# Kernel tuning notes

Measured on AMD Instinct MI355X. Metric: run time of the kernel, lower is better.

## Reference

```python
import jax, jax.numpy as jnp
from jax import lax
import numpy as np

PH, PW = 5, 5      # patch_shape; forced to 5x5 by the (batch, F, 27) reshape in AdaptiveConv
F = 32             # adaptive conv output channels
SCALE = 4          # super-resolution upscale factor


def conv2d(x, w, b, padding):
    # x: NCHW, w: OIHW
    y = lax.conv_general_dilated(x, w, (1, 1), padding,
                                 dimension_numbers=('NCHW', 'OIHW', 'NCHW'))
    return y + b[None, :, None, None]


def space_to_batch(x):
    # non-overlapping PHxPW tiles, order (batch, tile_row, tile_col) like the torch loops
    B, C, H, W = x.shape
    hn, wn = H // PH, W // PW
    p = x.reshape(B, C, hn, PH, wn, PW).transpose(0, 2, 4, 1, 3, 5)
    return p.reshape(B * hn * wn, C, PH, PW), (B, hn, wn)


def batch_to_space(p, meta):
    B, hn, wn = meta
    C = p.shape[1]
    out = p.reshape(B, hn, wn, C, PH, PW).transpose(0, 3, 1, 4, 2, 5)
    return out.reshape(B, C, hn * PH, wn * PW)


def unfold3(x):
    # torch F.unfold(x, 3, padding=1): (N, C*9, L) channel-major (c, kh, kw); return (N, L, C*9)
    N, C, H, W = x.shape
    xp = jnp.pad(x, ((0, 0), (0, 0), (1, 1), (1, 1)))
    cols = jnp.stack([xp[:, :, i:i + H, j:j + W]
                      for i in range(3) for j in range(3)], axis=2)  # (N, C, 9, H, W)
    return cols.reshape(N, C * 9, H * W).transpose(0, 2, 1)


def pixel_shuffle(x, r):
    B, Cr2, H, W = x.shape
    C = Cr2 // (r * r)
    return (x.reshape(B, C, r, r, H, W)
             .transpose(0, 1, 4, 2, 5, 3)
             .reshape(B, C, H * r, W * r))


def setup_inputs() -> dict:
    key = jax.random.key(0)
    ks = jax.random.split(key, 13)
    rn = lambda k, shape, s=0.05: jax.random.normal(k, shape, jnp.float32) * s
    return dict(
        x=jax.random.normal(ks[0], (2, 3, 360, 640), jnp.float32),
        w_feat=rn(ks[1], (256, 3, 3, 3)),        b_feat=rn(ks[2], (256,)),
        w_kern=rn(ks[3], (27 * F, 256, 3, 3)),   b_kern=rn(ks[4], (27 * F,)),
        w_badp=rn(ks[5], (F, 256, 3, 3)),        b_badp=rn(ks[6], (F,)),
        w1=rn(ks[7], (128, F, 5, 5)),            b1=rn(ks[8], (128,)),
        w2=rn(ks[9], (32, 128, 3, 3)),           b2=rn(ks[10], (32,)),
        w3=rn(ks[11], (3 * SCALE * SCALE, 32, 3, 3)), b3=rn(ks[12], (3 * SCALE * SCALE,)),
    )


def reference(x, w_feat, b_feat, w_kern, b_kern, w_badp, b_badp,
              w1, b1, w2, b2, w3, b3):
    patches, meta = space_to_batch(x)                        # (N, 3, 5, 5)
    N = patches.shape[0]
    # AdaptiveConv: per-patch dynamic 3x3 conv
    feat = jax.nn.relu(conv2d(patches, w_feat, b_feat, 'VALID'))   # (N, 256, 3, 3)
    kern = conv2d(feat, w_kern, b_kern, 'VALID')                   # (N, 27F, 1, 1)
    kern = kern.reshape(N, F, 27).transpose(0, 2, 1)               # (N, 27, F)
    xu = unfold3(patches)                                          # (N, 25, 27)
    out = jnp.einsum('nlk,nkf->nlf', xu, kern)                     # (N, 25, F)
    out = out.transpose(0, 2, 1).reshape(N, F, PH, PW)
    bias = conv2d(feat, w_badp, b_badp, 'VALID')                   # (N, F, 1, 1)
    out = jax.nn.relu(out + bias)
    sp = batch_to_space(out, meta)                                 # (B, F, H, W)
    # RegularConv stack
    h = jax.nn.relu(conv2d(sp, w1, b1, 'SAME'))
    h = jax.nn.relu(conv2d(h, w2, b2, 'SAME'))
    h = conv2d(h, w3, b3, 'SAME')                                  # (B, 3*r*r, H, W)
    return pixel_shuffle(h, SCALE)                                 # (B, 3, H*r, W*r)
```

## Files before the change

### kernel.cpp

```cpp
#include <hip/hip_runtime.h>
#include <stdint.h>

typedef unsigned short ushort;
typedef __bf16 bf16x8 __attribute__((ext_vector_type(8)));
typedef float f32x4 __attribute__((ext_vector_type(4)));
typedef ushort ushort8 __attribute__((ext_vector_type(8)));

__device__ __forceinline__ float bf2f(ushort u) {
  union { unsigned int i; float f; } v; v.i = ((unsigned int)u) << 16; return v.f;
}
__device__ __forceinline__ ushort f2bf(float f) {
  union { float f; unsigned int i; } v; v.f = f;
  unsigned int r = v.i + 0x7fffu + ((v.i >> 16) & 1u);
  return (ushort)(r >> 16);
}
__device__ __forceinline__ void glds16(const ushort* g, ushort* l) {
  __builtin_amdgcn_global_load_lds(
      (const __attribute__((address_space(1))) void*)g,
      (__attribute__((address_space(3))) void*)l, 16, 0, 0);
}

__global__ __launch_bounds__(256) void pack_kernel(
    const float* __restrict__ w_kern, const float* __restrict__ b_kern,
    const float* __restrict__ w_badp, const float* __restrict__ b_badp,
    ushort* __restrict__ Bt, float* __restrict__ bias896) {
  int idx = blockIdx.x * 256 + threadIdx.x;
  const int total = 896 * 2304;
  if (idx < total) {
    int o = idx / 2304, k = idx - o * 2304;
    int c = k & 255, pos = k >> 8;
    float v = (o < 864) ? w_kern[(o * 256 + c) * 9 + pos]
                        : w_badp[((o - 864) * 256 + c) * 9 + pos];
    Bt[idx] = f2bf(v);
  } else if (idx < total + 896) {
    int o = idx - total;
    bias896[o] = (o < 864) ? b_kern[o] : b_badp[o - 864];
  }
}

__global__ __launch_bounds__(256) void pack2_kernel(
    const float* __restrict__ w1, const float* __restrict__ w2,
    const float* __restrict__ w3, ushort* __restrict__ wp1,
    ushort* __restrict__ wp2, ushort* __restrict__ wp3) {
  int idx = blockIdx.x * 256 + threadIdx.x;
  if (idx < 102400) {
    int t = idx >> 12, rm = idx & 4095, o = rm >> 5, c = rm & 31;
    wp1[idx] = f2bf(w1[(o * 32 + c) * 25 + t]);
  } else if (idx < 102400 + 36864) {
    int j = idx - 102400;
    int t = j >> 12, rm = j & 4095, o = rm >> 7, c = rm & 127;
    wp2[j] = f2bf(w2[(o * 128 + c) * 9 + t]);
  } else if (idx < 102400 + 36864 + 13824) {
    int j = idx - 139264;
    int t = j / 1536, rm = j - t * 1536, o = rm >> 5, c = rm & 31;
    wp3[j] = f2bf(w3[(o * 32 + c) * 9 + t]);
  }
}

__global__ __launch_bounds__(256) void feat_kernel(
    const float* __restrict__ x, const float* __restrict__ w_feat,
    const float* __restrict__ b_feat, ushort* __restrict__ feat) {
  __shared__ float xp[4][3][5][5];
  const int t = threadIdx.x;
  const int n0 = blockIdx.x * 4;
  for (int e = t; e < 300; e += 256) {
    int p = e / 75, rem = e - p * 75;
    int ci = rem / 25, r = rem - ci * 25, i = r / 5, j = r - i * 5;
    int n = n0 + p;
    int b = n / 9216, ph = (n >> 7) % 72, pw = n & 127;
    xp[p][ci][i][j] = x[((b * 3 + ci) * 360 + ph * 5 + i) * 640 + pw * 5 + j];
  }
  float wf[27];
#pragma unroll
  for (int m = 0; m < 27; ++m) wf[m] = w_feat[t * 27 + m];
  const float bv = b_feat[t];
  __syncthreads();
  for (int p = 0; p < 4; ++p) {
    ushort* dst = feat + (size_t)(n0 + p) * 2304 + t;
#pragma unroll
    for (int pi = 0; pi < 3; ++pi)
#pragma unroll
      for (int pj = 0; pj < 3; ++pj) {
        float acc = bv;
#pragma unroll
        for (int ci = 0; ci < 3; ++ci)
#pragma unroll
          for (int ki = 0; ki < 3; ++ki)
#pragma unroll
            for (int kj = 0; kj < 3; ++kj)
              acc = fmaf(xp[p][ci][pi + ki][pj + kj], wf[ci * 9 + ki * 3 + kj], acc);
        dst[(pi * 3 + pj) * 256] = f2bf(fmaxf(acc, 0.f));
      }
  }
}

__global__ __launch_bounds__(256) void gemm_kernel(
    const ushort* __restrict__ A, const ushort* __restrict__ Bt,
    const float* __restrict__ bias, ushort* __restrict__ C) {
  const int K = 2304, N = 896;
  __shared__ __align__(16) ushort lA[128 * 32];
  __shared__ __align__(16) ushort lB[128 * 32];
  const int m0 = blockIdx.x * 128, n0 = blockIdx.y * 128;
  const int t = threadIdx.x;
  const int lane = t & 63, wave = t >> 6;
  const int wm = wave >> 1, wn = wave & 1;
  f32x4 acc[4][4] = {};
  const ushort* gA = A + (size_t)(m0 + (t >> 2)) * K + (t & 3) * 8;
  const ushort* gB = Bt + (size_t)(n0 + (t >> 2)) * K + (t & 3) * 8;
  ushort* dA0 = &lA[wave * 512];
  ushort* dA1 = &lA[2048 + wave * 512];
  ushort* dB0 = &lB[wave * 512];
  ushort* dB1 = &lB[2048 + wave * 512];
  const int aoff = (wm * 64 + (lane & 15)) * 32 + (lane >> 4) * 8;
  const int boff = (wn * 64 + (lane & 15)) * 32 + (lane >> 4) * 8;
  for (int kt = 0; kt < K; kt += 32) {
    __syncthreads();
    glds16(gA + kt, dA0);
    glds16(gA + 64 * K + kt, dA1);
    glds16(gB + kt, dB0);
    glds16(gB + 64 * K + kt, dB1);
    __syncthreads();
    bf16x8 af[4], bfr[4];
#pragma unroll
    for (int mi = 0; mi < 4; ++mi) {
      ushort8 tmp = *(const ushort8*)(&lA[aoff + mi * 512]);
      af[mi] = __builtin_bit_cast(bf16x8, tmp);
    }
#pragma unroll
    for (int ni = 0; ni < 4; ++ni) {
      ushort8 tmp = *(const ushort8*)(&lB[boff + ni * 512]);
      bfr[ni] = __builtin_bit_cast(bf16x8, tmp);
    }
#pragma unroll
    for (int mi = 0; mi < 4; ++mi)
#pragma unroll
      for (int ni = 0; ni < 4; ++ni)
        acc[mi][ni] = __builtin_amdgcn_mfma_f32_16x16x32_bf16(af[mi], bfr[ni], acc[mi][ni], 0, 0, 0);
  }
#pragma unroll
  for (int ni = 0; ni < 4; ++ni) {
    int col = n0 + wn * 64 + ni * 16 + (lane & 15);
    float bv = bias[col];
#pragma unroll
    for (int mi = 0; mi < 4; ++mi) {
      int row0 = m0 + wm * 64 + mi * 16 + (lane >> 4) * 4;
#pragma unroll
      for (int r = 0; r < 4; ++r)
        C[(size_t)(row0 + r) * N + col] = f2bf(acc[mi][ni][r] + bv);
    }
  }
}

__global__ __launch_bounds__(256) void apply_kernel(
    const float* __restrict__ x, const ushort* __restrict__ kernbias,
    ushort* __restrict__ sp) {
  __shared__ float xp[8][3][7][7];
  __shared__ ushort outl[8][32][25];
  const int t = threadIdx.x;
  const int n0 = blockIdx.x * 8;
  const int b = n0 / 9216, ph = (n0 >> 7) % 72, pw0 = n0 & 127;
  for (int e = t; e < 8 * 3 * 49; e += 256) ((float*)xp)[e] = 0.f;
  __syncthreads();
  for (int e = t; e < 600; e += 256) {
    int p = e / 75, rem = e - p * 75;
    int ci = rem / 25, r = rem - ci * 25, i = r / 5, j = r - i * 5;
    xp[p][ci][i + 1][j + 1] = x[((b * 3 + ci) * 360 + ph * 5 + i) * 640 + (pw0 + p) * 5 + j];
  }
  __syncthreads();
  const int p = t >> 5, f = t & 31;
  const int n = n0 + p;
  float kk[27];
#pragma unroll
  for (int k = 0; k < 27; ++k) kk[k] = bf2f(kernbias[(size_t)n * 896 + f * 27 + k]);
  const float bv = bf2f(kernbias[(size_t)n * 896 + 864 + f]);
  for (int l = 0; l < 25; ++l) {
    int li = l / 5, lj = l - li * 5;
    float s = bv;
#pragma unroll
    for (int k = 0; k < 27; ++k) {
      int ci = k / 9, rm = k - ci * 9, ki = rm / 3, kj = rm - ki * 3;
      s = fmaf(xp[p][ci][li + ki][lj + kj], kk[k], s);
    }
    outl[p][f][l] = f2bf(fmaxf(s, 0.f));
  }
  __syncthreads();
  for (int e = t; e < 6400; e += 256) {
    int f2 = e & 31;
    int idx = e >> 5;
    int i = idx / 40, c40 = idx - i * 40;
    int pp = c40 / 5, j = c40 - pp * 5;
    sp[(((size_t)b * 360 + ph * 5 + i) * 640 + pw0 * 5 + c40) * 32 + f2] = outl[pp][f2][i * 5 + j];
  }
}

__global__ __launch_bounds__(512) void conv1_kernel(
    const ushort* __restrict__ sp, const ushort* __restrict__ wp1,
    const float* __restrict__ b1, ushort* __restrict__ h1) {
  __shared__ ushort8 lin[8 * 4 * 69];
  const int t = threadIdx.x;
  const int lane = t & 63, wave = t >> 6;
  const int wh = wave >> 1, wn = wave & 1;
  const int w0 = blockIdx.x * 64, h0 = blockIdx.y * 4, b = blockIdx.z;
  for (int u = t; u < 8 * 4 * 68; u += 512) {
    int c8 = u & 3, rest = u >> 2;
    int wx = rest % 68, r = rest / 68;
    int gh = h0 - 2 + r, gw = w0 - 2 + wx;
    ushort8 v = {};
    if ((unsigned)gh < 360u && (unsigned)gw < 640u)
      v = *(const ushort8*)(sp + (((size_t)b * 360 + gh) * 640 + gw) * 32 + c8 * 8);
    lin[(r * 4 + c8) * 69 + wx] = v;
  }
  __syncthreads();
  f32x4 acc[4][4] = {};
  const int abase = (lane >> 4) * 69 + (lane & 15);
  const ushort* wbase = wp1 + (wn * 64 + (lane & 15)) * 32 + (lane >> 4) * 8;
#pragma unroll 1
  for (int ki = 0; ki < 5; ++ki) {
#pragma unroll
    for (int kj = 0; kj < 5; ++kj) {
      const int tap = ki * 5 + kj;
      bf16x8 bfr[4];
#pragma unroll
      for (int nf = 0; nf < 4; ++nf) {
        ushort8 tmp = *(const ushort8*)(wbase + (size_t)tap * 4096 + nf * 512);
        bfr[nf] = __builtin_bit_cast(bf16x8, tmp);
      }
      bf16x8 afr[4];
#pragma unroll
      for (int mf = 0; mf < 4; ++mf)
        afr[mf] = __builtin_bit_cast(bf16x8, lin[(wh + ki) * 276 + abase + mf * 16 + kj]);
#pragma unroll
      for (int mf = 0; mf < 4; ++mf)
#pragma unroll
        for (int nf = 0; nf < 4; ++nf)
          acc[mf][nf] = __builtin_amdgcn_mfma_f32_16x16x32_bf16(afr[mf], bfr[nf], acc[mf][nf], 0, 0, 0);
    }
  }
  const int h = h0 + wh;
#pragma unroll
  for (int nf = 0; nf < 4; ++nf) {
    int oc = wn * 64 + nf * 16 + (lane & 15);
    float bv = b1[oc];
#pragma unroll
    for (int mf = 0; mf < 4; ++mf) {
      int w = w0 + mf * 16 + ((lane >> 4) << 2);
      size_t base = (((size_t)b * 360 + h) * 640 + w) * 128 + oc;
#pragma unroll
      for (int r = 0; r < 4; ++r)
        h1[base + (size_t)r * 128] = f2bf(fmaxf(acc[mf][nf][r] + bv, 0.f));
    }
  }
}

__device__ __forceinline__ void c2_load(ushort8* stg, const ushort* __restrict__ h1,
                                        int t, int b, int h0, int w0, int cb) {
#pragma unroll
  for (int j = 0; j < 7; ++j) {
    int u = t + j * 256;
    ushort8 v = {};
    if (u < 1584) {
      int r = u / 264, rem = u - r * 264;
      int c8 = rem / 66, wx = rem - c8 * 66;
      int gh = h0 - 1 + r, gw = w0 - 1 + wx;
      if ((unsigned)gh < 360u && (unsigned)gw < 640u)
        v = *(const ushort8*)(h1 + (((size_t)b * 360 + gh) * 640 + gw) * 128 + cb * 32 + c8 * 8);
    }
    stg[j] = v;
  }
}
__device__ __forceinline__ void c2_write(const ushort8* stg, ushort8* buf, int t) {
#pragma unroll
  for (int j = 0; j < 7; ++j) {
    int u = t + j * 256;
    if (u < 1584) {
      int r = u / 264, rem = u - r * 264;
      int c8 = rem / 66, wx = rem - c8 * 66;
      buf[c8 * 414 + r * 69 + wx] = stg[j];
    }
  }
}
__device__ __forceinline__ void c2_compute(const ushort8* buf, const ushort* __restrict__ wp2,
                                           int cb, int wave, int lp, int lk, f32x4 acc[4][2]) {
#pragma unroll
  for (int ki = 0; ki < 3; ++ki) {
    const int rb = lk * 414 + (wave + ki) * 69;
#pragma unroll
    for (int kj = 0; kj < 3; ++kj) {
      const int tap = ki * 3 + kj;
      bf16x8 bfr[2];
#pragma unroll
      for (int nf = 0; nf < 2; ++nf) {
        ushort8 tmp = *(const ushort8*)(wp2 + tap * 4096 + nf * 2048 + lp * 128 + cb * 32 + lk * 8);
        bfr[nf] = __builtin_bit_cast(bf16x8, tmp);
      }
      bf16x8 afr[4];
#pragma unroll
      for (int mf = 0; mf < 4; ++mf)
        afr[mf] = __builtin_bit_cast(bf16x8, buf[rb + lp + mf * 16 + kj]);
#pragma unroll
      for (int mf = 0; mf < 4; ++mf)
#pragma unroll
        for (int nf = 0; nf < 2; ++nf)
          acc[mf][nf] = __builtin_amdgcn_mfma_f32_16x16x32_bf16(afr[mf], bfr[nf], acc[mf][nf], 0, 0, 0);
    }
  }
}

__global__ __launch_bounds__(256) void conv2_kernel(
    const ushort* __restrict__ h1, const ushort* __restrict__ wp2,
    const float* __restrict__ b2, ushort* __restrict__ h2) {
  __shared__ ushort8 lin[2][4 * 414];
  const int t = threadIdx.x;
  const int lane = t & 63, wave = t >> 6;
  const int lp = lane & 15, lk = lane >> 4;
  const int w0 = blockIdx.x * 64, h0 = blockIdx.y * 4, b = blockIdx.z;
  f32x4 acc[4][2] = {};
  ushort8 stg[7];
  c2_load(stg, h1, t, b, h0, w0, 0);
#pragma unroll
  for (int it = 0; it < 5; ++it) {
    __syncthreads();
    if (it < 4) c2_write(stg, lin[it & 1], t);
    if (it < 3) c2_load(stg, h1, t, b, h0, w0, it + 1);
    if (it >= 1) c2_compute(lin[(it - 1) & 1], wp2, it - 1, wave, lp, lk, acc);
  }
  const int h = h0 + wave;
#pragma unroll
  for (int nf = 0; nf < 2; ++nf) {
    int oc = nf * 16 + lp;
    float bv = b2[oc];
#pragma unroll
    for (int mf = 0; mf < 4; ++mf) {
      int w = w0 + mf * 16 + lk * 4;
      size_t base = (((size_t)b * 360 + h) * 640 + w) * 32 + oc;
#pragma unroll
      for (int r = 0; r < 4; ++r)
        h2[base + (size_t)r * 32] = f2bf(fmaxf(acc[mf][nf][r] + bv, 0.f));
    }
  }
}

__global__ __launch_bounds__(256) void conv3_kernel(
    const ushort* __restrict__ h2, const ushort* __restrict__ wp3,
    const float* __restrict__ b3, float* __restrict__ out) {
  __shared__ ushort8 lin[4 * 4 * 67];
  const int t = threadIdx.x;
  const int lane = t & 63, wave = t >> 6;
  const int wh = wave & 1, wm = wave >> 1;
  const int w0 = blockIdx.x * 64, h0 = blockIdx.y * 2, b = blockIdx.z;
  for (int u = t; u < 4 * 4 * 66; u += 256) {
    int c8 = u & 3, rest = u >> 2;
    int wx = rest % 66, r = rest / 66;
    int gh = h0 - 1 + r, gw = w0 - 1 + wx;
    ushort8 v = {};
    if (gh >= 0 && gh < 360 && gw >= 0 && gw < 640)
      v = *(const ushort8*)(h2 + (((size_t)b * 360 + gh) * 640 + gw) * 32 + c8 * 8);
    lin[(r * 4 + c8) * 67 + wx] = v;
  }
  __syncthreads();
  f32x4 acc[2][3] = {};
  const int abase = (lane >> 4) * 67 + wm * 32 + (lane & 15);
  const ushort* wbase = wp3 + ((lane & 15)) * 32 + (lane >> 4) * 8;
#pragma unroll 1
  for (int ki = 0; ki < 3; ++ki) {
#pragma unroll
    for (int kj = 0; kj < 3; ++kj) {
      const int tap = ki * 3 + kj;
      bf16x8 bfr[3];
#pragma unroll
      for (int nf = 0; nf < 3; ++nf) {
        ushort8 tmp = *(const ushort8*)(wbase + (size_t)tap * 1536 + nf * 512);
        bfr[nf] = __builtin_bit_cast(bf16x8, tmp);
      }
      bf16x8 afr[2];
#pragma unroll
      for (int mf = 0; mf < 2; ++mf)
        afr[mf] = __builtin_bit_cast(bf16x8, lin[(wh + ki) * 268 + abase + mf * 16 + kj]);
#pragma unroll
      for (int mf = 0; mf < 2; ++mf)
#pragma unroll
        for (int nf = 0; nf < 3; ++nf)
          acc[mf][nf] = __builtin_amdgcn_mfma_f32_16x16x32_bf16(afr[mf], bfr[nf], acc[mf][nf], 0, 0, 0);
    }
  }
  const int h = h0 + wh;
#pragma unroll
  for (int nf = 0; nf < 3; ++nf) {
    int oc = nf * 16 + (lane & 15);
    float bv = b3[oc];
    int c = oc >> 4, r1 = (oc >> 2) & 3, r2 = oc & 3;
#pragma unroll
    for (int mf = 0; mf < 2; ++mf) {
      int wb = w0 + wm * 32 + mf * 16 + ((lane >> 4) << 2);
#pragma unroll
      for (int r = 0; r < 4; ++r) {
        int w = wb + r;
        out[(((size_t)b * 3 + c) * 1440 + h * 4 + r1) * 2560 + (size_t)w * 4 + r2] =
            acc[mf][nf][r] + bv;
      }
    }
  }
}

extern "C" void kernel_launch(void* const* d_in, const int* in_sizes, int n_in,
                              void* d_out, int out_size, void* d_ws, size_t ws_size,
                              hipStream_t stream) {
  const float* x      = (const float*)d_in[0];
  const float* w_feat = (const float*)d_in[1];
  const float* b_feat = (const float*)d_in[2];
  const float* w_kern = (const float*)d_in[3];
  const float* b_kern = (const float*)d_in[4];
  const float* w_badp = (const float*)d_in[5];
  const float* b_badp = (const float*)d_in[6];
  const float* w1 = (const float*)d_in[7];
  const float* b1 = (const float*)d_in[8];
  const float* w2 = (const float*)d_in[9];
  const float* b2 = (const float*)d_in[10];
  const float* w3 = (const float*)d_in[11];
  const float* b3 = (const float*)d_in[12];

  char* ws = (char*)d_ws;
  ushort* feat     = (ushort*)(ws);
  ushort* h1       = (ushort*)(ws);
  ushort* kernbias = (ushort*)(ws + 117964800);
  ushort* h2       = (ushort*)(ws + 117964800);
  ushort* wp1      = (ushort*)(ws + 147456000);
  ushort* wp2      = (ushort*)(ws + 147660800);
  ushort* wp3      = (ushort*)(ws + 147734528);
  ushort* sp       = (ushort*)(ws + 150994944);
  ushort* Bt       = (ushort*)(ws + 180486144);
  float*  bias896  = (float*)(ws + 184614912);

  pack_kernel<<<(896 * 2304 + 896 + 255) / 256, 256, 0, stream>>>(
      w_kern, b_kern, w_badp, b_badp, Bt, bias896);
  feat_kernel<<<4608, 256, 0, stream>>>(x, w_feat, b_feat, feat);
  gemm_kernel<<<dim3(144, 7), 256, 0, stream>>>(feat, Bt, bias896, kernbias);
  apply_kernel<<<2304, 256, 0, stream>>>(x, kernbias, sp);
  pack2_kernel<<<598, 256, 0, stream>>>(w1, w2, w3, wp1, wp2, wp3);
  conv1_kernel<<<dim3(10, 90, 2), 512, 0, stream>>>(sp, wp1, b1, h1);
  conv2_kernel<<<dim3(10, 90, 2), 256, 0, stream>>>(h1, wp2, b2, h2);
  conv3_kernel<<<dim3(10, 180, 2), 256, 0, stream>>>(h2, wp3, b3, (float*)d_out);
}
```

Baseline: 514.6 us.

## Swap MFMA operands for vectorized epilogue stores and prefetch conv1 weights

The MFMA operand order in conv1, conv2 and conv3 is swapped so each lane's accumulator holds four consecutive output channels. The epilogues can then write packed 4-element bf16 or float4 stores with vectorized bias loads, replacing scattered scalar 2-byte and 4-byte stores. Conv1 also double-buffers its per-tap weight fragments in registers, prefetching the next tap's weights while the current tap's MFMAs run, to hide global load latency. This costs extra registers in conv1 and relies on the transposed accumulator layout matching the new index math.

```diff
diff --git a/kernel.cpp b/kernel.cpp
--- a/kernel.cpp
+++ b/kernel.cpp
@@ -5,6 +5,7 @@
 typedef __bf16 bf16x8 __attribute__((ext_vector_type(8)));
 typedef float f32x4 __attribute__((ext_vector_type(4)));
 typedef ushort ushort8 __attribute__((ext_vector_type(8)));
+typedef ushort us4 __attribute__((ext_vector_type(4)));
 
 __device__ __forceinline__ float bf2f(ushort u) {
   union { unsigned int i; float f; } v; v.i = ((unsigned int)u) << 16; return v.f;
@@ -18,6 +19,9 @@
   __builtin_amdgcn_global_load_lds(
       (const __attribute__((address_space(1))) void*)g,
       (__attribute__((address_space(3))) void*)l, 16, 0, 0);
+}
+__device__ __forceinline__ bf16x8 ldw(const ushort* p) {
+  return __builtin_bit_cast(bf16x8, *(const ushort8*)p);
 }
 
 __global__ __launch_bounds__(256) void pack_kernel(
@@ -212,42 +216,51 @@
   }
   __syncthreads();
   f32x4 acc[4][4] = {};
-  const int abase = (lane >> 4) * 69 + (lane & 15);
-  const ushort* wbase = wp1 + (wn * 64 + (lane & 15)) * 32 + (lane >> 4) * 8;
+  const int lp = lane & 15, lk = lane >> 4;
+  const int abase0 = lk * 69 + lp;
+  const ushort* wb = wp1 + (wn * 64 + lp) * 32 + lk * 8;
+
+  bf16x8 wc[4], wx_[4];
+#pragma unroll
+  for (int nf = 0; nf < 4; ++nf) wc[nf] = ldw(wb + nf * 512);
+
+  auto do_tap = [&](int tp, const bf16x8* wr) {
+    int ki = (tp * 13) >> 6, kj = tp - ki * 5;
+    int ab = (wh + ki) * 276 + abase0 + kj;
+    bf16x8 afr[4];
+#pragma unroll
+    for (int mf = 0; mf < 4; ++mf)
+      afr[mf] = __builtin_bit_cast(bf16x8, lin[ab + mf * 16]);
+#pragma unroll
+    for (int mf = 0; mf < 4; ++mf)
+#pragma unroll
+      for (int nf = 0; nf < 4; ++nf)
+        acc[mf][nf] = __builtin_amdgcn_mfma_f32_16x16x32_bf16(wr[nf], afr[mf], acc[mf][nf], 0, 0, 0);
+  };
+
 #pragma unroll 1
-  for (int ki = 0; ki < 5; ++ki) {
-#pragma unroll
-    for (int kj = 0; kj < 5; ++kj) {
-      const int tap = ki * 5 + kj;
-      bf16x8 bfr[4];
-#pragma unroll
-      for (int nf = 0; nf < 4; ++nf) {
-        ushort8 tmp = *(const ushort8*)(wbase + (size_t)tap * 4096 + nf * 512);
-        bfr[nf] = __builtin_bit_cast(bf16x8, tmp);
-      }
-      bf16x8 afr[4];
-#pragma unroll
-      for (int mf = 0; mf < 4; ++mf)
-        afr[mf] = __builtin_bit_cast(bf16x8, lin[(wh + ki) * 276 + abase + mf * 16 + kj]);
-#pragma unroll
-      for (int mf = 0; mf < 4; ++mf)
-#pragma unroll
-        for (int nf = 0; nf < 4; ++nf)
-          acc[mf][nf] = __builtin_amdgcn_mfma_f32_16x16x32_bf16(afr[mf], bfr[nf], acc[mf][nf], 0, 0, 0);
-    }
-  }
+  for (int tp = 0; tp < 24; tp += 2) {
+#pragma unroll
+    for (int nf = 0; nf < 4; ++nf) wx_[nf] = ldw(wb + (tp + 1) * 4096 + nf * 512);
+    do_tap(tp, wc);
+#pragma unroll
+    for (int nf = 0; nf < 4; ++nf) wc[nf] = ldw(wb + (tp + 2) * 4096 + nf * 512);
+    do_tap(tp + 1, wx_);
+  }
+  do_tap(24, wc);
+
   const int h = h0 + wh;
 #pragma unroll
   for (int nf = 0; nf < 4; ++nf) {
-    int oc = wn * 64 + nf * 16 + (lane & 15);
-    float bv = b1[oc];
+    const int oc0 = wn * 64 + nf * 16 + lk * 4;
+    f32x4 bv = *(const f32x4*)(b1 + oc0);
 #pragma unroll
     for (int mf = 0; mf < 4; ++mf) {
-      int w = w0 + mf * 16 + ((lane >> 4) << 2);
-      size_t base = (((size_t)b * 360 + h) * 640 + w) * 128 + oc;
-#pragma unroll
-      for (int r = 0; r < 4; ++r)
-        h1[base + (size_t)r * 128] = f2bf(fmaxf(acc[mf][nf][r] + bv, 0.f));
+      const int w = w0 + mf * 16 + lp;
+      us4 pk;
+#pragma unroll
+      for (int r = 0; r < 4; ++r) pk[r] = f2bf(fmaxf(acc[mf][nf][r] + bv[r], 0.f));
+      *(us4*)(&h1[(((size_t)b * 360 + h) * 640 + w) * 128 + oc0]) = pk;
     }
   }
 }
@@ -301,7 +314,7 @@
       for (int mf = 0; mf < 4; ++mf)
 #pragma unroll
         for (int nf = 0; nf < 2; ++nf)
-          acc[mf][nf] = __builtin_amdgcn_mfma_f32_16x16x32_bf16(afr[mf], bfr[nf], acc[mf][nf], 0, 0, 0);
+          acc[mf][nf] = __builtin_amdgcn_mfma_f32_16x16x32_bf16(bfr[nf], afr[mf], acc[mf][nf], 0, 0, 0);
     }
   }
 }
@@ -327,15 +340,15 @@
   const int h = h0 + wave;
 #pragma unroll
   for (int nf = 0; nf < 2; ++nf) {
-    int oc = nf * 16 + lp;
-    float bv = b2[oc];
+    const int oc0 = nf * 16 + lk * 4;
+    f32x4 bv = *(const f32x4*)(b2 + oc0);
 #pragma unroll
     for (int mf = 0; mf < 4; ++mf) {
-      int w = w0 + mf * 16 + lk * 4;
-      size_t base = (((size_t)b * 360 + h) * 640 + w) * 32 + oc;
-#pragma unroll
-      for (int r = 0; r < 4; ++r)
-        h2[base + (size_t)r * 32] = f2bf(fmaxf(acc[mf][nf][r] + bv, 0.f));
+      const int w = w0 + mf * 16 + lp;
+      us4 pk;
+#pragma unroll
+      for (int r = 0; r < 4; ++r) pk[r] = f2bf(fmaxf(acc[mf][nf][r] + bv[r], 0.f));
+      *(us4*)(&h2[(((size_t)b * 360 + h) * 640 + w) * 32 + oc0]) = pk;
     }
   }
 }
@@ -347,6 +360,7 @@
   const int t = threadIdx.x;
   const int lane = t & 63, wave = t >> 6;
   const int wh = wave & 1, wm = wave >> 1;
+  const int lp = lane & 15, lk = lane >> 4;
   const int w0 = blockIdx.x * 64, h0 = blockIdx.y * 2, b = blockIdx.z;
   for (int u = t; u < 4 * 4 * 66; u += 256) {
     int c8 = u & 3, rest = u >> 2;
@@ -359,8 +373,8 @@
   }
   __syncthreads();
   f32x4 acc[2][3] = {};
-  const int abase = (lane >> 4) * 67 + wm * 32 + (lane & 15);
-  const ushort* wbase = wp3 + ((lane & 15)) * 32 + (lane >> 4) * 8;
+  const int abase = lk * 67 + wm * 32 + lp;
+  const ushort* wbase = wp3 + lp * 32 + lk * 8;
 #pragma unroll 1
   for (int ki = 0; ki < 3; ++ki) {
 #pragma unroll
@@ -380,24 +394,20 @@
       for (int mf = 0; mf < 2; ++mf)
 #pragma unroll
         for (int nf = 0; nf < 3; ++nf)
-          acc[mf][nf] = __builtin_amdgcn_mfma_f32_16x16x32_bf16(afr[mf], bfr[nf], acc[mf][nf], 0, 0, 0);
+          acc[mf][nf] = __builtin_amdgcn_mfma_f32_16x16x32_bf16(bfr[nf], afr[mf], acc[mf][nf], 0, 0, 0);
     }
   }
   const int h = h0 + wh;
 #pragma unroll
   for (int nf = 0; nf < 3; ++nf) {
-    int oc = nf * 16 + (lane & 15);
-    float bv = b3[oc];
-    int c = oc >> 4, r1 = (oc >> 2) & 3, r2 = oc & 3;
+    f32x4 bv = *(const f32x4*)(b3 + nf * 16 + lk * 4);
 #pragma unroll
     for (int mf = 0; mf < 2; ++mf) {
-      int wb = w0 + wm * 32 + mf * 16 + ((lane >> 4) << 2);
-#pragma unroll
-      for (int r = 0; r < 4; ++r) {
-        int w = wb + r;
-        out[(((size_t)b * 3 + c) * 1440 + h * 4 + r1) * 2560 + (size_t)w * 4 + r2] =
-            acc[mf][nf][r] + bv;
-      }
+      const int w = w0 + wm * 32 + mf * 16 + lp;
+      f32x4 o;
+#pragma unroll
+      for (int r = 0; r < 4; ++r) o[r] = acc[mf][nf][r] + bv[r];
+      *(f32x4*)(&out[(((size_t)b * 3 + nf) * 1440 + h * 4 + lk) * 2560 + (size_t)w * 4]) = o;
     }
   }
 }
```

Result: no change. 512.3 us (-0.4%).
